# Optimization experiments

Measured on AMD Instinct MI355X. Metric: run time of the kernel, lower is better.

The kernel has to match this reference:

```python
import jax, jax.numpy as jnp
import numpy as np

K = 512
H = 8
B = 8
T = 1024
EPS = 1e-5


def _layernorm(x, g, b):
    mu = jnp.mean(x, axis=-1, keepdims=True)
    var = jnp.var(x, axis=-1, keepdims=True)
    return (x - mu) * jax.lax.rsqrt(var + EPS) * g + b


def _attention(x, enc, wq, wk, wv, wo):
    b, t, k = x.shape
    h = H
    scale = k ** (-0.25)
    q = (x @ wq).reshape(b, t, h, k) * scale        # [b,t,h,k]
    kk = (enc @ wk).reshape(b, t, h, k) * scale
    v = (enc @ wv).reshape(b, t, h, k)
    dot = jnp.einsum('bqhd,bkhd->bhqk', q, kk)      # [b,h,t,t]
    att = jax.nn.softmax(dot, axis=-1)
    out = jnp.einsum('bhqk,bkhd->bqhd', att, v).reshape(b, t, h * k)
    return out @ wo                                  # [b,t,k]


def setup_inputs() -> dict:
    key = jax.random.key(0)
    ks = jax.random.split(key, 12)
    s = 0.02
    return {
        'x': jax.random.normal(ks[0], (B, T, K), jnp.float32),
        'enc': jax.random.normal(ks[1], (B, T, K), jnp.float32),
        'sa_wq': jax.random.normal(ks[2], (K, K * H), jnp.float32) * s,
        'sa_wk': jax.random.normal(ks[3], (K, K * H), jnp.float32) * s,
        'sa_wv': jax.random.normal(ks[4], (K, K * H), jnp.float32) * s,
        'sa_wo': jax.random.normal(ks[5], (K * H, K), jnp.float32) * s,
        'ca_wq': jax.random.normal(ks[6], (K, K * H), jnp.float32) * s,
        'ca_wk': jax.random.normal(ks[7], (K, K * H), jnp.float32) * s,
        'ca_wv': jax.random.normal(ks[8], (K, K * H), jnp.float32) * s,
        'ca_wo': jax.random.normal(ks[9], (K * H, K), jnp.float32) * s,
        'ln1_g': jnp.ones((K,), jnp.float32), 'ln1_b': jnp.zeros((K,), jnp.float32),
        'ln2_g': jnp.ones((K,), jnp.float32), 'ln2_b': jnp.zeros((K,), jnp.float32),
        'ln3_g': jnp.ones((K,), jnp.float32), 'ln3_b': jnp.zeros((K,), jnp.float32),
        'ff_w1': jax.random.normal(ks[10], (K, 4 * K), jnp.float32) * s,
        'ff_b1': jnp.zeros((4 * K,), jnp.float32),
        'ff_w2': jax.random.normal(ks[11], (4 * K, K), jnp.float32) * s,
        'ff_b2': jnp.zeros((K,), jnp.float32),
    }


def reference(x, enc, sa_wq, sa_wk, sa_wv, sa_wo, ca_wq, ca_wk, ca_wv, ca_wo,
              ln1_g, ln1_b, ln2_g, ln2_b, ln3_g, ln3_b,
              ff_w1, ff_b1, ff_w2, ff_b2):
    # masked self-attention (mask_future_steps=False -> plain self-attn)
    sa = _attention(x, x, sa_wq, sa_wk, sa_wv, sa_wo)
    x = _layernorm(sa + x, ln1_g, ln1_b)
    # encoder-decoder attention
    ca = _attention(x, enc, ca_wq, ca_wk, ca_wv, ca_wo)
    x = _layernorm(ca + x, ln2_g, ln2_b)
    # dropout p=0.0 -> identity
    ff = jax.nn.relu(x @ ff_w1 + ff_b1) @ ff_w2 + ff_b2
    x = _layernorm(ff + x, ln3_g, ln3_b)
    return x
```

## Files before the change

### kernel.cpp

```cpp
#include <hip/hip_runtime.h>
#include <stdint.h>

typedef short short8 __attribute__((ext_vector_type(8)));
typedef float f32x4 __attribute__((ext_vector_type(4)));
typedef unsigned short us4 __attribute__((ext_vector_type(4)));

#define DEVI static __device__ __forceinline__

DEVI float b2f(unsigned short u) {
  union { float f; uint32_t i; } v; v.i = ((uint32_t)u) << 16; return v.f;
}
DEVI unsigned short f2b(float f) {
  union { float f; uint32_t i; } v; v.f = f;
  uint32_t r = v.i + 0x7FFFu + ((v.i >> 16) & 1u);
  return (unsigned short)(r >> 16);
}

DEVI void async_cp16(const unsigned short* g, unsigned short* l) {
  __builtin_amdgcn_global_load_lds(
      (const __attribute__((address_space(1))) void*)g,
      (__attribute__((address_space(3))) void*)l, 16, 0, 0);
}

DEVI void swz(int& bx, int& by, int& bz) {
  const int gx = gridDim.x, gy = gridDim.y, gz = gridDim.z;
  int l = blockIdx.x + gx * (blockIdx.y + gy * blockIdx.z);
  bz = l % gz; l /= gz;
  by = l % gy;
  bx = l / gy;
}


__global__ __launch_bounds__(256) void cvt_f32_bf16(
    const float4* __restrict__ src, unsigned short* __restrict__ dst) {
  const int i = blockIdx.x * 256 + threadIdx.x;
  float4 f = src[i];
  uint2 o;
  o.x = (uint32_t)f2b(f.x) | ((uint32_t)f2b(f.y) << 16);
  o.y = (uint32_t)f2b(f.z) | ((uint32_t)f2b(f.w) << 16);
  ((uint2*)dst)[i] = o;
}

__global__ __launch_bounds__(256) void wtrans(
    const float* __restrict__ src, unsigned short* __restrict__ dst, int R, int C) {
  __shared__ float tile[32][33];
  const int tx = threadIdx.x & 31, ty = threadIdx.x >> 5;
  const int c0 = blockIdx.x * 32, r0 = blockIdx.y * 32;
#pragma unroll
  for (int i = 0; i < 32; i += 8)
    tile[ty + i][tx] = src[(long)(r0 + ty + i) * C + c0 + tx];
  __syncthreads();
#pragma unroll
  for (int i = 0; i < 32; i += 8)
    dst[(long)(c0 + ty + i) * R + r0 + tx] = f2b(tile[tx][ty + i]);
}

__global__ __launch_bounds__(256) void softmax_rows(
    unsigned short* __restrict__ S, int NZ) {
  const int tid = threadIdx.x;
  const int bx = blockIdx.x;
  const long z = bx % NZ, r = bx / NZ;
  unsigned short* p = S + (z * 1024 + r) * 1024;
  us4 raw = ((const us4*)p)[tid];
  float v[4];
  float m = -3.0e38f;
#pragma unroll
  for (int i = 0; i < 4; i++) { v[i] = b2f(raw[i]); m = fmaxf(m, v[i]); }
#pragma unroll
  for (int o = 1; o < 64; o <<= 1) m = fmaxf(m, __shfl_xor(m, o));
  __shared__ float rm[4], rsum[4];
  const int lane = tid & 63, wave = tid >> 6;
  if (lane == 0) rm[wave] = m;
  __syncthreads();
  m = fmaxf(fmaxf(rm[0], rm[1]), fmaxf(rm[2], rm[3]));
  float s = 0.f;
#pragma unroll
  for (int i = 0; i < 4; i++) { v[i] = __expf(v[i] - m); s += v[i]; }
#pragma unroll
  for (int o = 1; o < 64; o <<= 1) s += __shfl_xor(s, o);
  if (lane == 0) rsum[wave] = s;
  __syncthreads();
  s = rsum[0] + rsum[1] + rsum[2] + rsum[3];
  const float inv = 1.f / s;
  us4 out;
#pragma unroll
  for (int i = 0; i < 4; i++) out[i] = f2b(v[i] * inv);
  ((us4*)p)[tid] = out;
}

__global__ __launch_bounds__(256) void layernorm_rows(
    const float* X, const float* __restrict__ g,
    const float* __restrict__ b, float* Y,
    unsigned short* __restrict__ Yb) {
  const int tid = threadIdx.x;
  const long row = blockIdx.x;
  const float* x = X + row * 512;
  float v0 = x[tid], v1 = x[tid + 256];
  float s1 = v0 + v1;
  float s2 = v0 * v0 + v1 * v1;
#pragma unroll
  for (int o = 1; o < 64; o <<= 1) {
    s1 += __shfl_xor(s1, o);
    s2 += __shfl_xor(s2, o);
  }
  __shared__ float r1[4], r2[4];
  const int lane = tid & 63, wave = tid >> 6;
  if (lane == 0) { r1[wave] = s1; r2[wave] = s2; }
  __syncthreads();
  s1 = r1[0] + r1[1] + r1[2] + r1[3];
  s2 = r2[0] + r2[1] + r2[2] + r2[3];
  const float mu = s1 * (1.f / 512.f);
  const float var = s2 * (1.f / 512.f) - mu * mu;
  const float rs = rsqrtf(var + 1e-5f);
  float y0 = (v0 - mu) * rs * g[tid] + b[tid];
  float y1 = (v1 - mu) * rs * g[tid + 256] + b[tid + 256];
  if (Y) { Y[row * 512 + tid] = y0; Y[row * 512 + tid + 256] = y1; }
  if (Yb) { Yb[row * 512 + tid] = f2b(y0); Yb[row * 512 + tid + 256] = f2b(y1); }
}

template <int EPI, int BM>
__global__ __launch_bounds__(256, 2) void gemm_bt(
    const unsigned short* __restrict__ A, int lda, long asb, long ash,
    const unsigned short* __restrict__ B, int ldb, long bsb, long bsh,
    void* Cv, int ldc, long csb, long csh,
    int K, float scale,
    const float* __restrict__ bias, const float* res) {
  constexpr int MI = BM / 32;
  __shared__ __align__(16) unsigned short As[2][BM * 32];
  __shared__ __align__(16) unsigned short Bs[2][128 * 32];
  int bx, by, bz;
  swz(bx, by, bz);
  const int tid = threadIdx.x;
  const int lane = tid & 63;
  const int wave = tid >> 6;
  const int zb = bz >> 3, zh = bz & 7;
  const int m0 = by * BM;
  const int n0 = bx * 128;

  const unsigned short* Ab = A + zb * asb + zh * ash + (long)m0 * lda;
  const unsigned short* Bb = B + zb * bsb + zh * bsh + (long)n0 * ldb;

  const int r0 = tid >> 2;
  const int p0 = (((tid & 3) ^ ((r0 >> 1) & 3)) << 3);

  f32x4 acc[MI][4];
#pragma unroll
  for (int i = 0; i < MI; i++)
#pragma unroll
    for (int j = 0; j < 4; j++) acc[i][j] = (f32x4){0.f, 0.f, 0.f, 0.f};

  const int wm = (wave >> 1) * (BM / 2);
  const int wn = (wave & 1) << 6;
  const int fm = lane & 15;
  const int k8 = (lane >> 4) << 3;

  auto stage = [&](int buf, int kt) {
    if constexpr (BM == 128) {
      async_cp16(Ab + (long)r0 * lda + kt + p0, &As[buf][tid * 8]);
      async_cp16(Ab + (long)(r0 + 64) * lda + kt + p0, &As[buf][2048 + tid * 8]);
    } else if constexpr (BM == 64) {
      async_cp16(Ab + (long)r0 * lda + kt + p0, &As[buf][tid * 8]);
    } else {
      if (tid < 128) async_cp16(Ab + (long)r0 * lda + kt + p0, &As[buf][tid * 8]);
    }
    async_cp16(Bb + (long)r0 * ldb + kt + p0, &Bs[buf][tid * 8]);
    async_cp16(Bb + (long)(r0 + 64) * ldb + kt + p0, &Bs[buf][2048 + tid * 8]);
  };
  auto sidx = [&](int row) { return row * 32 + (k8 ^ (((row >> 1) & 3) << 3)); };

  const int nt = K >> 5;
  stage(0, 0);
  __syncthreads();
  int cur = 0;
  for (int t = 0; t < nt; ++t) {
    if (t + 1 < nt) stage(cur ^ 1, (t + 1) << 5);

    short8 af[MI], bfr[4];
#pragma unroll
    for (int i = 0; i < MI; i++)
      af[i] = *(const short8*)&As[cur][sidx(wm + i * 16 + fm)];
#pragma unroll
    for (int j = 0; j < 4; j++)
      bfr[j] = *(const short8*)&Bs[cur][sidx(wn + j * 16 + fm)];
#pragma unroll
    for (int i = 0; i < MI; i++)
#pragma unroll
      for (int j = 0; j < 4; j++)
        acc[i][j] = __builtin_amdgcn_mfma_f32_16x16x32_bf16(af[i], bfr[j], acc[i][j], 0, 0, 0);

    __syncthreads();
    cur ^= 1;
  }

  const long coff = zb * csb + zh * csh;
  const int er = (lane >> 4) << 2;
  const int ec = lane & 15;
#pragma unroll
  for (int i = 0; i < MI; i++) {
#pragma unroll
    for (int j = 0; j < 4; j++) {
      const int gc = n0 + wn + j * 16 + ec;
#pragma unroll
      for (int r = 0; r < 4; r++) {
        const int gr = m0 + wm + i * 16 + er + r;
        const float v = acc[i][j][r];
        const long idx = coff + (long)gr * ldc + gc;
        if constexpr (EPI == 0) {
          ((unsigned short*)Cv)[idx] = f2b(v * scale);
        } else if constexpr (EPI == 1) {
          float o = v;
          if (bias) o += bias[gc];
          if (res) o += res[(long)gr * ldc + gc];
          ((float*)Cv)[idx] = o;
        } else {
          ((unsigned short*)Cv)[idx] = f2b(fmaxf(v + bias[gc], 0.f));
        }
      }
    }
  }
}

extern "C" void kernel_launch(void* const* d_in, const int* in_sizes, int n_in,
                              void* d_out, int out_size, void* d_ws, size_t ws_size,
                              hipStream_t stream) {
  const float* x     = (const float*)d_in[0];
  const float* enc   = (const float*)d_in[1];
  const float* ln1_g = (const float*)d_in[10];
  const float* ln1_b = (const float*)d_in[11];
  const float* ln2_g = (const float*)d_in[12];
  const float* ln2_b = (const float*)d_in[13];
  const float* ln3_g = (const float*)d_in[14];
  const float* ln3_b = (const float*)d_in[15];
  const float* ff_b1 = (const float*)d_in[17];
  const float* ff_b2 = (const float*)d_in[19];

  uint8_t* ws = (uint8_t*)d_ws;
  auto US = [&](size_t o) { return (unsigned short*)(ws + o); };
  auto F  = [&](size_t o) { return (float*)(ws + o); };

  const size_t MB = 1ull << 20;
  const size_t SZ_WBIG = 4 * MB, SZ_WFF = 2 * MB;

  const size_t O_XB = 0, O_ENCB = 8 * MB, O_WT = 16 * MB;
  const size_t O_RES = 52 * MB;
  const size_t O_XNB = 68 * MB;
  auto WT = [&](int i) { return US(O_WT + (size_t)i * SZ_WBIG); };

  int HP = 1;
  for (int c = 8; c >= 1; c >>= 1)
    if (ws_size >= (76 + 40 * (size_t)c) * MB) { HP = c; break; }
  const int NG = 8 / HP;
  const int NZ = HP * 8;
  const int LD = HP * 512;
  const size_t O_QG  = 76 * MB;
  const size_t O_KG  = O_QG + (size_t)HP * 8 * MB;
  const size_t O_VTG = O_KG + (size_t)HP * 8 * MB;
  const size_t O_SG  = O_VTG + (size_t)HP * 8 * MB;
  const size_t O_H   = 76 * MB;

  const float qsc = 0.21022410381342863f;
  dim3 B256(256);

  cvt_f32_bf16<<<4096, B256, 0, stream>>>((const float4*)x, US(O_XB));
  cvt_f32_bf16<<<4096, B256, 0, stream>>>((const float4*)enc, US(O_ENCB));

  struct WSpec { const float* s; size_t off; int R, C; };
  const WSpec wspec[10] = {
      {(const float*)d_in[2], O_WT + 0 * SZ_WBIG, 512, 4096},
      {(const float*)d_in[3], O_WT + 1 * SZ_WBIG, 512, 4096},
      {(const float*)d_in[4], O_WT + 2 * SZ_WBIG, 512, 4096},
      {(const float*)d_in[5], O_WT + 3 * SZ_WBIG, 4096, 512},
      {(const float*)d_in[6], O_WT + 4 * SZ_WBIG, 512, 4096},
      {(const float*)d_in[7], O_WT + 5 * SZ_WBIG, 512, 4096},
      {(const float*)d_in[8], O_WT + 6 * SZ_WBIG, 512, 4096},
      {(const float*)d_in[9], O_WT + 7 * SZ_WBIG, 4096, 512},
      {(const float*)d_in[16], O_WT + 8 * SZ_WBIG, 512, 2048},
      {(const float*)d_in[18], O_WT + 8 * SZ_WBIG + SZ_WFF, 2048, 512},
  };
  for (int i = 0; i < 10; i++)
    wtrans<<<dim3(wspec[i].C / 32, wspec[i].R / 32), B256, 0, stream>>>(
        wspec[i].s, US(wspec[i].off), wspec[i].R, wspec[i].C);

  auto attention = [&](const unsigned short* qsrc, const unsigned short* kvsrc,
                       int wb, const float* resid) {
    for (int g = 0; g < NG; g++) {
      const size_t woff = (size_t)g * LD * 512;
      gemm_bt<0, 128><<<dim3(HP * 4, 64, 1), B256, 0, stream>>>(
          qsrc, 512, 0, 0, WT(wb + 0) + woff, 512, 0, 0,
          US(O_QG), LD, 0, 0, 512, qsc, nullptr, nullptr);
      gemm_bt<0, 128><<<dim3(HP * 4, 64, 1), B256, 0, stream>>>(
          kvsrc, 512, 0, 0, WT(wb + 1) + woff, 512, 0, 0,
          US(O_KG), LD, 0, 0, 512, qsc, nullptr, nullptr);
      gemm_bt<0, 128><<<dim3(64, HP * 4, 1), B256, 0, stream>>>(
          WT(wb + 2) + woff, 512, 0, 0, kvsrc, 512, 0, 0,
          US(O_VTG), 8192, 0, 0, 512, 1.f, nullptr, nullptr);
      gemm_bt<0, 128><<<dim3(8, 8, NZ), B256, 0, stream>>>(
          US(O_QG), LD, 512L, (long)1024 * LD,
          US(O_KG), LD, 512L, (long)1024 * LD,
          US(O_SG), 1024, 8388608L, 1048576L, 512, 1.f, nullptr, nullptr);
      softmax_rows<<<NZ * 1024, B256, 0, stream>>>(US(O_SG), NZ);
      gemm_bt<0, 128><<<dim3(4, 8, NZ), B256, 0, stream>>>(
          US(O_SG), 1024, 8388608L, 1048576L,
          US(O_VTG), 8192, 4194304L, 1024L,
          US(O_QG), LD, 512L, (long)1024 * LD, 1024, 1.f, nullptr, nullptr);
      gemm_bt<1, 32><<<dim3(4, 256, 1), B256, 0, stream>>>(
          US(O_QG), LD, 0, 0, WT(wb + 3) + (size_t)g * LD, 4096, 0, 0,
          F(O_RES), 512, 0, 0, LD, 1.f, nullptr, g == 0 ? resid : F(O_RES));
    }
  };

  attention(US(O_XB), US(O_XB), 0, x);
  layernorm_rows<<<8192, B256, 0, stream>>>(F(O_RES), ln1_g, ln1_b, F(O_RES), US(O_XNB));
  attention(US(O_XNB), US(O_ENCB), 4, F(O_RES));
  layernorm_rows<<<8192, B256, 0, stream>>>(F(O_RES), ln2_g, ln2_b, F(O_RES), US(O_XNB));
  gemm_bt<2, 128><<<dim3(16, 64, 1), B256, 0, stream>>>(
      US(O_XNB), 512, 0, 0, WT(8), 512, 0, 0,
      US(O_H), 2048, 0, 0, 512, 1.f, ff_b1, nullptr);
  gemm_bt<1, 32><<<dim3(4, 256, 1), B256, 0, stream>>>(
      US(O_H), 2048, 0, 0, US(O_WT + 8 * SZ_WBIG + SZ_WFF), 2048, 0, 0,
      F(O_RES), 512, 0, 0, 2048, 1.f, ff_b2, F(O_RES));
  layernorm_rows<<<8192, B256, 0, stream>>>(F(O_RES), ln3_g, ln3_b, (float*)d_out, nullptr);
}
```

Measured before the change: 1.280 ms.

## Split-K output projections with atomic accumulation into pre-seeded residual

```diff
diff --git a/kernel.cpp b/kernel.cpp
--- a/kernel.cpp
+++ b/kernel.cpp
@@ -53,6 +53,16 @@
 #pragma unroll
   for (int i = 0; i < 32; i += 8)
     dst[(long)(c0 + ty + i) * R + r0 + tx] = f2b(tile[tx][ty + i]);
+}
+
+__global__ __launch_bounds__(256) void seed_rows(
+    float* __restrict__ dst, const float* src, const float* bias) {
+  const int tid = threadIdx.x;
+  const long row = blockIdx.x;
+  float v0 = src[row * 512 + tid], v1 = src[row * 512 + tid + 256];
+  if (bias) { v0 += bias[tid]; v1 += bias[tid + 256]; }
+  dst[row * 512 + tid] = v0;
+  dst[row * 512 + tid + 256] = v1;
 }
 
 __global__ __launch_bounds__(256) void softmax_rows(
@@ -137,8 +147,16 @@
   const int m0 = by * BM;
   const int n0 = bx * 128;
 
-  const unsigned short* Ab = A + zb * asb + zh * ash + (long)m0 * lda;
-  const unsigned short* Bb = B + zb * bsb + zh * bsh + (long)n0 * ldb;
+  long aoff, boff;
+  if constexpr (EPI == 3) {
+    aoff = (long)bz * asb;
+    boff = (long)bz * bsb;
+  } else {
+    aoff = zb * asb + zh * ash;
+    boff = zb * bsb + zh * bsh;
+  }
+  const unsigned short* Ab = A + aoff + (long)m0 * lda;
+  const unsigned short* Bb = B + boff + (long)n0 * ldb;
 
   const int r0 = tid >> 2;
   const int p0 = (((tid & 3) ^ ((r0 >> 1) & 3)) << 3);
@@ -155,14 +173,9 @@
   const int k8 = (lane >> 4) << 3;
 
   auto stage = [&](int buf, int kt) {
-    if constexpr (BM == 128) {
-      async_cp16(Ab + (long)r0 * lda + kt + p0, &As[buf][tid * 8]);
+    async_cp16(Ab + (long)r0 * lda + kt + p0, &As[buf][tid * 8]);
+    if constexpr (BM == 128)
       async_cp16(Ab + (long)(r0 + 64) * lda + kt + p0, &As[buf][2048 + tid * 8]);
-    } else if constexpr (BM == 64) {
-      async_cp16(Ab + (long)r0 * lda + kt + p0, &As[buf][tid * 8]);
-    } else {
-      if (tid < 128) async_cp16(Ab + (long)r0 * lda + kt + p0, &As[buf][tid * 8]);
-    }
     async_cp16(Bb + (long)r0 * ldb + kt + p0, &Bs[buf][tid * 8]);
     async_cp16(Bb + (long)(r0 + 64) * ldb + kt + p0, &Bs[buf][2048 + tid * 8]);
   };
@@ -192,7 +205,7 @@
     cur ^= 1;
   }
 
-  const long coff = zb * csb + zh * csh;
+  const long coff = (EPI == 3) ? 0 : (zb * csb + zh * csh);
   const int er = (lane >> 4) << 2;
   const int ec = lane & 15;
 #pragma unroll
@@ -212,8 +225,10 @@
           if (bias) o += bias[gc];
           if (res) o += res[(long)gr * ldc + gc];
           ((float*)Cv)[idx] = o;
+        } else if constexpr (EPI == 2) {
+          ((unsigned short*)Cv)[idx] = f2b(fmaxf(v + bias[gc], 0.f));
         } else {
-          ((unsigned short*)Cv)[idx] = f2b(fmaxf(v + bias[gc], 0.f));
+          atomicAdd(&((float*)Cv)[idx], v);
         }
       }
     }
@@ -283,6 +298,8 @@
 
   auto attention = [&](const unsigned short* qsrc, const unsigned short* kvsrc,
                        int wb, const float* resid) {
+    if (resid != F(O_RES))
+      seed_rows<<<8192, B256, 0, stream>>>(F(O_RES), resid, nullptr);
     for (int g = 0; g < NG; g++) {
       const size_t woff = (size_t)g * LD * 512;
       gemm_bt<0, 128><<<dim3(HP * 4, 64, 1), B256, 0, stream>>>(
@@ -303,9 +320,9 @@
           US(O_SG), 1024, 8388608L, 1048576L,
           US(O_VTG), 8192, 4194304L, 1024L,
           US(O_QG), LD, 512L, (long)1024 * LD, 1024, 1.f, nullptr, nullptr);
-      gemm_bt<1, 32><<<dim3(4, 256, 1), B256, 0, stream>>>(
-          US(O_QG), LD, 0, 0, WT(wb + 3) + (size_t)g * LD, 4096, 0, 0,
-          F(O_RES), 512, 0, 0, LD, 1.f, nullptr, g == 0 ? resid : F(O_RES));
+      gemm_bt<3, 64><<<dim3(4, 128, 4), B256, 0, stream>>>(
+          US(O_QG), LD, LD / 4, 0, WT(wb + 3) + (size_t)g * LD, 4096, LD / 4, 0,
+          F(O_RES), 512, 0, 0, LD / 4, 1.f, nullptr, nullptr);
     }
   };
 
@@ -316,8 +333,9 @@
   gemm_bt<2, 128><<<dim3(16, 64, 1), B256, 0, stream>>>(
       US(O_XNB), 512, 0, 0, WT(8), 512, 0, 0,
       US(O_H), 2048, 0, 0, 512, 1.f, ff_b1, nullptr);
-  gemm_bt<1, 32><<<dim3(4, 256, 1), B256, 0, stream>>>(
-      US(O_H), 2048, 0, 0, US(O_WT + 8 * SZ_WBIG + SZ_WFF), 2048, 0, 0,
-      F(O_RES), 512, 0, 0, 2048, 1.f, ff_b2, F(O_RES));
+  seed_rows<<<8192, B256, 0, stream>>>(F(O_RES), F(O_RES), ff_b2);
+  gemm_bt<3, 64><<<dim3(4, 128, 4), B256, 0, stream>>>(
+      US(O_H), 2048, 512, 0, US(O_WT + 8 * SZ_WBIG + SZ_WFF), 2048, 512, 0,
+      F(O_RES), 512, 0, 0, 512, 1.f, nullptr, nullptr);
   layernorm_rows<<<8192, B256, 0, stream>>>(F(O_RES), ln3_g, ln3_b, (float*)d_out, nullptr);
 }
```

Result: slower. 1.373 ms (+7.3%).
